# Performance work log

Measured on AMD Instinct MI355X. Metric: run time of the kernel, lower is better.

The kernel has to match this reference:

```python
import jax, jax.numpy as jnp
import numpy as np

N_OFFSETS = 72            # number of y-rows a lane proposal is sampled at (LaneATT)
N_STRIPS = N_OFFSETS - 1  # 71
IMG_W = 640.0             # nominal image width for x coordinates


def setup_inputs() -> dict:
    key = jax.random.key(0)
    k1, k2 = jax.random.split(key)
    n = 8192
    raw = jax.random.uniform(k1, (n, 2 + 3 + N_OFFSETS), dtype=jnp.float32)
    # LaneATT proposal layout: [score0, score1, start_y, start_x, length, xs(72)]
    start_y = raw[:, 2]                      # normalized [0,1]
    start_x = raw[:, 3] * IMG_W
    length = raw[:, 4] * N_STRIPS            # length in strips
    xs = raw[:, 5:] * IMG_W                  # x coords in pixels
    proposals = jnp.concatenate(
        [raw[:, :2], start_y[:, None], start_x[:, None], length[:, None], xs], axis=1
    )
    scores = jax.random.uniform(k2, (n,), dtype=jnp.float32)
    return {"proposals": proposals, "scores": scores, "nms_thres": 50, "nms_topk": 8}


def _line_nms(proposals, scores, nms_thres, nms_topk):
    """Greedy line NMS over lane proposals (LaneATT semantics)."""
    n = proposals.shape[0]
    order = jnp.argsort(-scores)
    p = proposals[order]                                   # [n, 77] sorted by score desc
    starts = jnp.round(p[:, 2] * N_STRIPS).astype(jnp.int32)       # [n]
    ends = jnp.minimum(starts + jnp.round(p[:, 4]).astype(jnp.int32) - 1, N_STRIPS)
    xs = p[:, 5:]                                          # [n, 72]
    k_idx = jnp.arange(N_OFFSETS)
    thr = jnp.float32(nms_thres)

    # suppression matrix row-by-row via lax.map to bound peak memory
    def supp_row(args):
        xi, si, ei = args
        ps = jnp.maximum(si, starts)                       # [n] pairwise overlap start
        pe = jnp.minimum(ei, ends)                         # [n] pairwise overlap end
        valid = (k_idx[None, :] >= ps[:, None]) & (k_idx[None, :] <= pe[:, None])
        d = jnp.sum(jnp.where(valid, jnp.abs(xi[None, :] - xs), 0.0), axis=1)
        cnt = jnp.maximum(pe - ps + 1, 1).astype(jnp.float32)
        return (pe >= ps) & (d / cnt < thr)                # [n] bool

    S = jax.lax.map(supp_row, (xs, starts, ends))          # [n, n] bool

    # sequential greedy pass: keep highest-score lane, suppress its neighbors
    def step(removed, inp):
        s_row, i = inp
        alive = ~removed[i]
        removed = removed | (alive & s_row)
        return removed, alive

    _, keep = jax.lax.scan(step, jnp.zeros((n,), bool), (S, jnp.arange(n)))

    rank = jnp.cumsum(keep)
    sel = keep & (rank <= nms_topk)
    idx = jnp.where(sel, size=nms_topk, fill_value=n)[0]   # padded with n (zero row)
    p_pad = jnp.concatenate([p, jnp.zeros((1, p.shape[1]), p.dtype)], axis=0)
    s_pad = jnp.concatenate([scores[order], jnp.zeros((1,), scores.dtype)], axis=0)
    kept = jnp.concatenate([p_pad[idx], s_pad[idx][:, None]], axis=1)  # [topk, 78]
    num_kept = jnp.minimum(jnp.sum(keep), nms_topk)
    return kept, num_kept


def reference(proposals, scores, nms_thres, nms_topk):
    return _line_nms(proposals, scores, nms_thres, nms_topk)
```

## Files before the change

### kernel.cpp

```cpp
#include <hip/hip_runtime.h>


#define NTH     256
#define SLOTS   32
#define NWAVES  (NTH / 64)
#define N_OFF   72
#define NSTRIP  71
#define PROW    77
#define MAXK    8
#define CANDMAX 64
#define PRE     16

__device__ __forceinline__ unsigned long long pack_key(float s, int idx) {
    return ((unsigned long long)__float_as_uint(s) << 32) |
           (unsigned long long)(0xFFFFFFFFu - (unsigned)idx);
}
__device__ __forceinline__ int key_idx(unsigned long long k) {
    return (int)(0xFFFFFFFFu - (unsigned)(k & 0xFFFFFFFFu));
}

__device__ __forceinline__ unsigned long long bitonic64_desc(
        unsigned long long v, int lane) {
#pragma unroll
    for (int k = 2; k <= 64; k <<= 1) {
#pragma unroll
        for (int j = k >> 1; j > 0; j >>= 1) {
            unsigned long long pv = __shfl_xor(v, j);
            bool lower   = (lane & j) == 0;
            bool dirdesc = (lane & k) != 0;
            bool keepmax = (dirdesc != lower);
            unsigned long long mx = v > pv ? v : pv;
            unsigned long long mn = v > pv ? pv : v;
            v = keepmax ? mx : mn;
        }
    }
    return v;
}

__global__ __launch_bounds__(NTH, 1) void lane_nms(
    const float* __restrict__ prop,
    const float* __restrict__ scores,
    const int* __restrict__ p_thres,
    const int* __restrict__ p_topk,
    float* __restrict__ out,
    int n, int out_rows)
{
    const int tid  = threadIdx.x;
    const int lane = tid & 63;
    const int wv   = tid >> 6;

    __shared__ unsigned long long s_wmax[NWAVES];
    __shared__ unsigned long long s_tmax[NTH];
    __shared__ unsigned long long s_cand[CANDMAX];
    __shared__ unsigned long long s_thr64;
    __shared__ unsigned long long s_resume;
    __shared__ float s_rows[PRE][PROW + 1];
    __shared__ float s_buf[2][PROW + 1];
    __shared__ float s_kxs[MAXK][N_OFF];
    __shared__ int   s_ks[MAXK], s_ke[MAXK];
    __shared__ int   s_sup[2];
    __shared__ int   s_cnt, s_kept, s_fb;

    const float thr = (float)(*p_thres);
    int topk = *p_topk;
    if (topk > out_rows) topk = out_rows;
    if (topk > MAXK)     topk = MAXK;

    unsigned long long key[SLOTS];
#pragma unroll
    for (int jo = 0; jo < SLOTS / 4; ++jo) {
        int base = jo * (NTH * 4) + tid * 4;
        if (base + 3 < n) {
            const float4 s4 = *reinterpret_cast<const float4*>(scores + base);
            key[jo * 4 + 0] = pack_key(s4.x, base + 0);
            key[jo * 4 + 1] = pack_key(s4.y, base + 1);
            key[jo * 4 + 2] = pack_key(s4.z, base + 2);
            key[jo * 4 + 3] = pack_key(s4.w, base + 3);
        } else {
#pragma unroll
            for (int c = 0; c < 4; ++c) {
                int idx = base + c;
                key[jo * 4 + c] = (idx < n) ? pack_key(scores[idx], idx) : 0ULL;
            }
        }
    }
    unsigned long long tmax = 0ULL;
#pragma unroll
    for (int j = 0; j < SLOTS; ++j)
        if (key[j] > tmax) tmax = key[j];

    s_tmax[tid] = tmax;
    if (tid == 0) { s_cnt = 0; s_sup[0] = 0; s_sup[1] = 0; }
    __syncthreads();

    if (wv == 0) {
        unsigned long long g = s_tmax[lane * 4 + 0];
        unsigned long long t1 = s_tmax[lane * 4 + 1]; if (t1 > g) g = t1;
        unsigned long long t2 = s_tmax[lane * 4 + 2]; if (t2 > g) g = t2;
        unsigned long long t3 = s_tmax[lane * 4 + 3]; if (t3 > g) g = t3;
        g = bitonic64_desc(g, lane);
        if (lane == 15) s_thr64 = g;
    }
    __syncthreads();
    const unsigned long long T = s_thr64;

#pragma unroll
    for (int j = 0; j < SLOTS; ++j) {
        unsigned long long k = key[j];
        if (k != 0ULL && k >= T) {
            int pos = atomicAdd(&s_cnt, 1);
            if (pos < CANDMAX) s_cand[pos] = k;
        }
    }
    __syncthreads();
    const int  cnt  = s_cnt;
    const bool fast = (cnt <= CANDMAX) && (topk > 0);

    int kept = 0;
    bool fb = (topk > 0);
    unsigned long long resume = ~0ULL;

    if (fast) {
        const int ncand = cnt;
        if (wv == 0) {
            unsigned long long v = (lane < ncand) ? s_cand[lane] : 0ULL;
            v = bitonic64_desc(v, lane);
            s_cand[lane] = v;
        }
        __syncthreads();

        const int npre = ncand < PRE ? ncand : PRE;
        for (int i = tid; i < npre * (PROW + 1); i += NTH) {
            int r = i / (PROW + 1), c = i - r * (PROW + 1);
            int w = key_idx(s_cand[r]);
            s_rows[r][c] = (c < PROW) ? prop[(size_t)w * PROW + c] : scores[w];
        }
        __syncthreads();

        if (wv == 0) {
            int  pref = npre;
            int  k0 = 0;
            bool hit_topk = false;
            for (int c = 0; c < ncand; ++c) {
                if (c >= pref) {
                    int w = key_idx(s_cand[c]);
                    for (int i = lane; i < PROW + 1; i += 64)
                        s_rows[c & (PRE - 1)][i] =
                            (i < PROW) ? prop[(size_t)w * PROW + i] : scores[w];
                    asm volatile("s_waitcnt lgkmcnt(0)" ::: "memory");
                    pref = c + 1;
                }
                const int slot = c & (PRE - 1);
                float sy = s_rows[slot][2];
                float ln = s_rows[slot][4];
                int cs = (int)rintf(sy * (float)NSTRIP);
                int ce = cs + (int)rintf(ln) - 1;
                if (ce > NSTRIP) ce = NSTRIP;

                bool pred = false;
                {
                    int j = lane >> 3, l = lane & 7;
                    if (j < k0) {
                        int ps = cs > s_ks[j] ? cs : s_ks[j];
                        int pe = ce < s_ke[j] ? ce : s_ke[j];
                        if (pe >= ps) {
                            float d = 0.0f;
                            for (int k = ps + l; k <= pe; k += 8)
                                d += fabsf(s_rows[slot][5 + k] - s_kxs[j][k]);
                            d += __shfl_down(d, 4, 8);
                            d += __shfl_down(d, 2, 8);
                            d += __shfl_down(d, 1, 8);
                            if (l == 0 && d / (float)(pe - ps + 1) < thr)
                                pred = true;
                        }
                    }
                }
                if (__ballot((int)pred) == 0ULL) {
                    for (int i = lane; i < PROW + 1; i += 64)
                        out[k0 * (PROW + 1) + i] = s_rows[slot][i];
                    for (int i = lane; i < N_OFF; i += 64)
                        s_kxs[k0][i] = s_rows[slot][5 + i];
                    if (lane == 0) { s_ks[k0] = cs; s_ke[k0] = ce; }
                    ++k0;
                    if (k0 >= topk) { hit_topk = true; break; }
                    asm volatile("s_waitcnt lgkmcnt(0)" ::: "memory");
                }
            }
            if (lane == 0) {
                s_kept   = k0;
                s_fb     = (!hit_topk && k0 < topk) ? 1 : 0;
                s_resume = (ncand > 0) ? s_cand[ncand - 1] : 0ULL;
            }
        }
        __syncthreads();
        kept   = s_kept;
        fb     = (s_fb != 0);
        resume = s_resume;
    }

    if (fb && kept < topk) {
        auto scan = [&](unsigned long long lim) {
            unsigned long long m = 0ULL;
#pragma unroll
            for (int j = 0; j < SLOTS; ++j) {
                unsigned long long k = key[j];
                if (k < lim && k > m) m = k;
            }
#pragma unroll
            for (int off = 32; off > 0; off >>= 1) {
                unsigned long long o = __shfl_down(m, off);
                if (o > m) m = o;
            }
            if (lane == 0) s_wmax[wv] = m;
        };
        auto merge = [&]() {
            unsigned long long m = s_wmax[0];
#pragma unroll
            for (int i = 1; i < NWAVES; ++i)
                if (s_wmax[i] > m) m = s_wmax[i];
            return m;
        };

        scan(resume);
        __syncthreads();
        unsigned long long k1 = merge();
        __syncthreads();
        scan(k1);
        __syncthreads();
        unsigned long long k2 = merge();

        if (k1 != 0ULL) {
            int w = key_idx(k1);
            if (tid < PROW)       s_buf[0][tid]  = prop[(size_t)w * PROW + tid];
            else if (tid == PROW) s_buf[0][PROW] = scores[w];
        }
        if (k2 != 0ULL) {
            int w = key_idx(k2);
            if (tid >= NTH - PROW - 1) {
                int t = tid - (NTH - PROW - 1);
                s_buf[1][t] = (t < PROW) ? prop[(size_t)w * PROW + t] : scores[w];
            }
        }
        __syncthreads();

        int p = 0, q = 0;
        unsigned long long curk = k1, nxtk = k2;
        while (curk != 0ULL) {
            scan(nxtk);
            float sy = s_buf[p][2];
            float ln = s_buf[p][4];
            int cs = (int)rintf(sy * (float)NSTRIP);
            int ce = cs + (int)rintf(ln) - 1;
            if (ce > NSTRIP) ce = NSTRIP;
            if (tid < kept) {
                int ps = cs > s_ks[tid] ? cs : s_ks[tid];
                int pe = ce < s_ke[tid] ? ce : s_ke[tid];
                if (pe >= ps) {
                    float d = 0.0f;
                    for (int k = ps; k <= pe; ++k)
                        d += fabsf(s_buf[p][5 + k] - s_kxs[tid][k]);
                    if (d / (float)(pe - ps + 1) < thr) s_sup[q] = 1;
                }
            }
            if (tid == NTH - 1) s_sup[q ^ 1] = 0;
            __syncthreads();

            unsigned long long k3 = merge();
            if (s_sup[q] == 0) {
                if (tid < PROW + 1) out[kept * (PROW + 1) + tid] = s_buf[p][tid];
                if (tid < N_OFF)    s_kxs[kept][tid] = s_buf[p][5 + tid];
                if (tid == 0) { s_ks[kept] = cs; s_ke[kept] = ce; }
                ++kept;
                if (kept >= topk) break;
            }
            __syncthreads();

            if (k3 != 0ULL) {
                int w = key_idx(k3);
                if (tid < PROW)       s_buf[p][tid]  = prop[(size_t)w * PROW + tid];
                else if (tid == PROW) s_buf[p][PROW] = scores[w];
            }
            curk = nxtk; nxtk = k3; p ^= 1; q ^= 1;
        }
    }

    for (int i = tid; i < (out_rows - kept) * (PROW + 1); i += NTH)
        out[kept * (PROW + 1) + i] = 0.0f;
    if (tid == 0) out[out_rows * (PROW + 1)] = (float)kept;
}

extern "C" void kernel_launch(void* const* d_in, const int* in_sizes, int n_in,
                              void* d_out, int out_size, void* d_ws, size_t ws_size,
                              hipStream_t stream) {
    const float* prop   = (const float*)d_in[0];
    const float* scores = (const float*)d_in[1];
    const int*   thres  = (const int*)d_in[2];
    const int*   topk   = (const int*)d_in[3];
    int n        = in_sizes[1];
    int out_rows = (out_size - 1) / (PROW + 1);
    lane_nms<<<1, NTH, 0, stream>>>(prop, scores, thres, topk,
                                    (float*)d_out, n, out_rows);
}
```

Baseline: 73.58 us.

## Compute pairwise suppression bitmask in parallel for top-16 candidates before greedy pass

Replaces the single-wave sequential greedy loop over candidates with a block-parallel pairwise suppression matrix over the first 16 prefetched candidates, stored as 32-bit bitmasks. A single thread then runs the greedy keep/suppress pass over those bitmasks, and the kept rows are written out cooperatively. Candidates beyond the first 16 are no longer handled in the fast path and fall back to the general scan, which can add fallback work when fewer than topk lanes survive among the first 16.

```diff
diff --git a/kernel.cpp b/kernel.cpp
--- a/kernel.cpp
+++ b/kernel.cpp
@@ -59,6 +59,8 @@
     __shared__ float s_kxs[MAXK][N_OFF];
     __shared__ int   s_ks[MAXK], s_ke[MAXK];
     __shared__ int   s_sup[2];
+    __shared__ unsigned int s_sup32[PRE];
+    __shared__ int   s_keptidx[MAXK];
     __shared__ int   s_cnt, s_kept, s_fb;
 
     const float thr = (float)(*p_thres);
@@ -130,6 +132,7 @@
         __syncthreads();
 
         const int npre = ncand < PRE ? ncand : PRE;
+        if (tid < PRE) s_sup32[tid] = 0u;
         for (int i = tid; i < npre * (PROW + 1); i += NTH) {
             int r = i / (PROW + 1), c = i - r * (PROW + 1);
             int w = key_idx(s_cand[r]);
@@ -137,65 +140,66 @@
         }
         __syncthreads();
 
-        if (wv == 0) {
-            int  pref = npre;
-            int  k0 = 0;
-            bool hit_topk = false;
-            for (int c = 0; c < ncand; ++c) {
-                if (c >= pref) {
-                    int w = key_idx(s_cand[c]);
-                    for (int i = lane; i < PROW + 1; i += 64)
-                        s_rows[c & (PRE - 1)][i] =
-                            (i < PROW) ? prop[(size_t)w * PROW + i] : scores[w];
-                    asm volatile("s_waitcnt lgkmcnt(0)" ::: "memory");
-                    pref = c + 1;
+        {
+            int i = tid >> 4, j = tid & 15;
+            if (i < j && j < npre) {
+                float syi = s_rows[i][2], lni = s_rows[i][4];
+                int csi = (int)rintf(syi * (float)NSTRIP);
+                int cei = csi + (int)rintf(lni) - 1;
+                if (cei > NSTRIP) cei = NSTRIP;
+                float syj = s_rows[j][2], lnj = s_rows[j][4];
+                int csj = (int)rintf(syj * (float)NSTRIP);
+                int cej = csj + (int)rintf(lnj) - 1;
+                if (cej > NSTRIP) cej = NSTRIP;
+                int ps = csi > csj ? csi : csj;
+                int pe = cei < cej ? cei : cej;
+                if (pe >= ps) {
+                    float d = 0.0f;
+                    for (int k = ps; k <= pe; ++k)
+                        d += fabsf(s_rows[i][5 + k] - s_rows[j][5 + k]);
+                    if (d / (float)(pe - ps + 1) < thr)
+                        atomicOr(&s_sup32[i], 1u << j);
                 }
-                const int slot = c & (PRE - 1);
-                float sy = s_rows[slot][2];
-                float ln = s_rows[slot][4];
+            }
+        }
+        __syncthreads();
+
+        if (tid == 0) {
+            unsigned removed = 0u;
+            int k0 = 0;
+            for (int i = 0; i < npre && k0 < topk; ++i) {
+                if (!((removed >> i) & 1u)) {
+                    s_keptidx[k0++] = i;
+                    removed |= s_sup32[i];
+                }
+            }
+            s_kept   = k0;
+            s_fb     = (k0 < topk) ? 1 : 0;
+            s_resume = (npre > 0) ? s_cand[npre - 1] : 0ULL;
+        }
+        __syncthreads();
+        kept   = s_kept;
+        fb     = (s_fb != 0);
+        resume = s_resume;
+
+        for (int i = tid; i < kept * (PROW + 1); i += NTH) {
+            int kk = i / (PROW + 1), c = i - kk * (PROW + 1);
+            out[i] = s_rows[s_keptidx[kk]][c];
+        }
+        if (fb) {
+            for (int i = tid; i < kept * N_OFF; i += NTH) {
+                int kk = i / N_OFF, c = i - kk * N_OFF;
+                s_kxs[kk][c] = s_rows[s_keptidx[kk]][5 + c];
+            }
+            if (tid < kept) {
+                int slot = s_keptidx[tid];
+                float sy = s_rows[slot][2], ln = s_rows[slot][4];
                 int cs = (int)rintf(sy * (float)NSTRIP);
                 int ce = cs + (int)rintf(ln) - 1;
                 if (ce > NSTRIP) ce = NSTRIP;
-
-                bool pred = false;
-                {
-                    int j = lane >> 3, l = lane & 7;
-                    if (j < k0) {
-                        int ps = cs > s_ks[j] ? cs : s_ks[j];
-                        int pe = ce < s_ke[j] ? ce : s_ke[j];
-                        if (pe >= ps) {
-                            float d = 0.0f;
-                            for (int k = ps + l; k <= pe; k += 8)
-                                d += fabsf(s_rows[slot][5 + k] - s_kxs[j][k]);
-                            d += __shfl_down(d, 4, 8);
-                            d += __shfl_down(d, 2, 8);
-                            d += __shfl_down(d, 1, 8);
-                            if (l == 0 && d / (float)(pe - ps + 1) < thr)
-                                pred = true;
-                        }
-                    }
-                }
-                if (__ballot((int)pred) == 0ULL) {
-                    for (int i = lane; i < PROW + 1; i += 64)
-                        out[k0 * (PROW + 1) + i] = s_rows[slot][i];
-                    for (int i = lane; i < N_OFF; i += 64)
-                        s_kxs[k0][i] = s_rows[slot][5 + i];
-                    if (lane == 0) { s_ks[k0] = cs; s_ke[k0] = ce; }
-                    ++k0;
-                    if (k0 >= topk) { hit_topk = true; break; }
-                    asm volatile("s_waitcnt lgkmcnt(0)" ::: "memory");
-                }
-            }
-            if (lane == 0) {
-                s_kept   = k0;
-                s_fb     = (!hit_topk && k0 < topk) ? 1 : 0;
-                s_resume = (ncand > 0) ? s_cand[ncand - 1] : 0ULL;
-            }
-        }
-        __syncthreads();
-        kept   = s_kept;
-        fb     = (s_fb != 0);
-        resume = s_resume;
+                s_ks[tid] = cs; s_ke[tid] = ce;
+            }
+        }
     }
 
     if (fb && kept < topk) {
```

Measured after the change: 70.85 us. -3.7%, faster.
